# Kernel optimization log

Hardware: AMD Instinct MI355X
Metric: run time of the kernel (lower is better)

Reference implementation:

```python
import jax, jax.numpy as jnp
import numpy as np

MAX_ITERS = 20
TOL = 1e-6
STEP = 1.0
EPS = 1e-7
CLIP = 1e-7


def _normalize(x, axis=-1):
    n = jnp.linalg.norm(x, axis=axis, keepdims=True)
    return x / jnp.maximum(n, 1e-12)


def _safe_acos(x):
    return jnp.arccos(jnp.clip(x, -1.0 + CLIP, 1.0 - CLIP))


def setup_inputs() -> dict:
    key = jax.random.key(0)
    NC, K, N, D = 1000, 8, 32, 128
    X_groups = jax.random.normal(key, (NC, K, N, D), dtype=jnp.float32)
    return {"X_groups": X_groups}


def reference(X_groups):
    # X_groups: (NC, K, N, D)
    NC, K, N, D = X_groups.shape
    X = X_groups.reshape(NC * K, N, D)
    Xn = _normalize(X)                      # (G, N, D) unit vectors
    mu = _normalize(jnp.mean(Xn, axis=1))   # (G, D) init mean

    done = jnp.array(False)
    for _ in range(MAX_ITERS):
        dots = jnp.einsum('gd,gnd->gn', mu, Xn)             # (G, N)
        theta = _safe_acos(dots)
        sin_t = jnp.maximum(jnp.sin(theta), EPS)
        diff = Xn - dots[..., None] * mu[:, None, :]        # (G, N, D)
        log_vecs = (theta / sin_t)[..., None] * diff        # log map
        v = jnp.mean(log_vecs, axis=1)                      # (G, D)
        v_norm = jnp.maximum(jnp.linalg.norm(v, axis=-1, keepdims=True), EPS)
        done = done | (jnp.max(v_norm) < TOL)               # global convergence (as in torch .item() check)
        v_step = STEP * v
        vs_norm = jnp.maximum(jnp.linalg.norm(v_step, axis=-1, keepdims=True), EPS)
        mu_new = jnp.cos(vs_norm) * mu + jnp.sin(vs_norm) * (v_step / vs_norm)  # exp map
        mu_new = _normalize(mu_new)
        mu = jnp.where(done, mu, mu_new)

    # calc_cluster_distance: features (G, N, D) @ means (G, D)
    sims = jnp.einsum('gnd,gd->gn', Xn, mu)
    sims = jnp.clip(sims, -1 + CLIP, 1 - CLIP)
    loss = jnp.mean(jnp.sum(jnp.arccos(sims) ** 2, axis=-1))
    return loss
```

## Files before the change

kernel.cpp:

```cpp
#include <hip/hip_runtime.h>
#include <stdint.h>

#define MAX_ITERS 20
#define EPSV 1e-7f
#define CLIPV 1e-7f
#define PI_F 3.14159265358979f
#define PIO2_F 1.57079632679490f

typedef __attribute__((ext_vector_type(8))) short short8;
typedef __attribute__((ext_vector_type(4))) float f4;

__device__ __forceinline__ f4 mfma_bf16(short8 a, short8 b, f4 c) {
    return __builtin_amdgcn_mfma_f32_16x16x32_bf16(a, b, c, 0, 0, 0);
}

__device__ __forceinline__ float rl(float v, int l) {
    return __int_as_float(__builtin_amdgcn_readlane(__float_as_int(v), l));
}

template <int CTRL>
__device__ __forceinline__ float dpp_add(float v) {
    int p = __builtin_amdgcn_update_dpp(0, __float_as_int(v), CTRL, 0xF, 0xF, true);
    return v + __int_as_float(p);
}

__device__ __forceinline__ float rowsum32(float v) {
    v = dpp_add<0xB1>(v);
    v = dpp_add<0x4E>(v);
    v = dpp_add<0x141>(v);
    v = dpp_add<0x140>(v);
    return rl(v, 0) + rl(v, 16);
}

__device__ __forceinline__ float fast_acos(float x) {
    float a = fabsf(x);
    bool big = a > 0.5f;
    float z = big ? 0.5f * (1.0f - a) : x * x;
    float s = big ? sqrtf(z) : x;
    float p = fmaf(z, fmaf(z, fmaf(z, fmaf(z, 4.2163199048e-2f, 2.4181311049e-2f),
                                   4.5470025998e-2f), 7.4953002686e-2f),
                   1.6666752422e-1f);
    float r = fmaf(s * z, p, s);
    float big_val = (x < 0.0f) ? (PI_F - 2.0f * r) : (2.0f * r);
    return big ? big_val : (PIO2_F - r);
}

__device__ __forceinline__ void cvt_hilo(const float* v, short8& hi, short8& lo) {
#pragma unroll
    for (int i = 0; i < 8; ++i) {
        float x = v[i];
        uint32_t u = __float_as_uint(x);
        float hf = __uint_as_float(u & 0xFFFF0000u);
        float lf = x - hf;
        hi[i] = (short)(u >> 16);
        lo[i] = (short)(__float_as_uint(lf) >> 16);
    }
}

__global__ void __launch_bounds__(256) karcher(const float* __restrict__ X,
                                               float* __restrict__ ws,
                                               int n_groups) {
    __shared__ float sG[4][32 * 33];
    __shared__ float sInv[4][32];
    __shared__ float sPart[4];

    const int lane = threadIdx.x & 63;
    const int wid  = threadIdx.x >> 6;
    const int g    = blockIdx.x * 4 + wid;
    if (g >= n_groups) return;

    const float* Xg = X + (size_t)g * (32 * 128);
    const int col  = lane & 15;
    const int quad = lane >> 4;

    f4 acc00 = {0.f, 0.f, 0.f, 0.f};
    f4 acc01 = acc00, acc10 = acc00, acc11 = acc00;
#pragma unroll
    for (int kc = 0; kc < 4; ++kc) {
        const float* p0 = Xg + col * 128 + kc * 32 + quad * 8;
        const float* p1 = p0 + 16 * 128;
        float r0[8], r1[8];
        *(float4*)(r0)     = *(const float4*)(p0);
        *(float4*)(r0 + 4) = *(const float4*)(p0 + 4);
        *(float4*)(r1)     = *(const float4*)(p1);
        *(float4*)(r1 + 4) = *(const float4*)(p1 + 4);
        short8 H0, L0, H1, L1;
        cvt_hilo(r0, H0, L0);
        cvt_hilo(r1, H1, L1);
        acc00 = mfma_bf16(H0, H0, acc00);
        acc00 = mfma_bf16(H0, L0, acc00);
        acc00 = mfma_bf16(L0, H0, acc00);
        acc01 = mfma_bf16(H0, H1, acc01);
        acc01 = mfma_bf16(H0, L1, acc01);
        acc01 = mfma_bf16(L0, H1, acc01);
        acc10 = mfma_bf16(H1, H0, acc10);
        acc10 = mfma_bf16(H1, L0, acc10);
        acc10 = mfma_bf16(L1, H0, acc10);
        acc11 = mfma_bf16(H1, H1, acc11);
        acc11 = mfma_bf16(H1, L1, acc11);
        acc11 = mfma_bf16(L1, H1, acc11);
    }

    float* Gw = sG[wid];
#pragma unroll
    for (int i = 0; i < 4; ++i) {
        int rw = quad * 4 + i;
        Gw[rw * 33 + col]             = acc00[i];
        Gw[rw * 33 + col + 16]        = acc01[i];
        Gw[(rw + 16) * 33 + col]      = acc10[i];
        Gw[(rw + 16) * 33 + col + 16] = acc11[i];
    }
    __syncthreads();

    const int r = lane & 31;
    {
        float d = Gw[r * 33 + r];
        sInv[wid][r] = 1.0f / fmaxf(sqrtf(d), 1e-12f);
    }
    __syncthreads();

    float Grow[32];
    {
        float invr = sInv[wid][r];
#pragma unroll
        for (int j = 0; j < 32; ++j)
            Grow[j] = Gw[r * 33 + j] * (invr * sInv[wid][j]);
    }

    float a = 1.0f / 32.0f;
    float ga;
    {
        float s0 = 0, s1 = 0, s2 = 0, s3 = 0;
#pragma unroll
        for (int j = 0; j < 8; ++j) {
            s0 += Grow[j];
            s1 += Grow[j + 8];
            s2 += Grow[j + 16];
            s3 += Grow[j + 24];
        }
        ga = ((s0 + s1) + (s2 + s3)) * (1.0f / 32.0f);
        float n2   = rowsum32(a * ga);
        float inv0 = 1.0f / fmaxf(sqrtf(n2), 1e-12f);
        a  *= inv0;
        ga *= inv0;
    }

    for (int it = 0; it < MAX_ITERS; ++it) {
        float x  = fminf(fmaxf(ga, -1.0f + CLIPV), 1.0f - CLIPV);
        float th = fast_acos(x);
        float st = fmaxf(sqrtf(fmaxf(1.0f - x * x, 0.0f)), EPSV);
        float w  = __fdividef(th, st);
        float C  = rowsum32(w * ga);
        float beta = (w - C * a) * (1.0f / 32.0f);
        float gb0 = 0, gb1 = 0, gb2 = 0, gb3 = 0;
#pragma unroll
        for (int j = 0; j < 8; ++j) {
            gb0 = fmaf(Grow[j],      rl(beta, j),      gb0);
            gb1 = fmaf(Grow[j + 8],  rl(beta, j + 8),  gb1);
            gb2 = fmaf(Grow[j + 16], rl(beta, j + 16), gb2);
            gb3 = fmaf(Grow[j + 24], rl(beta, j + 24), gb3);
        }
        float gb = (gb0 + gb1) + (gb2 + gb3);
        float vv = rowsum32(beta * gb);
        float vs = fmaxf(sqrtf(fmaxf(vv, 0.0f)), EPSV);
        float cv = __cosf(vs);
        float sv = __fdividef(__sinf(vs), vs);
        a  = fmaf(sv, beta, cv * a);
        ga = fmaf(sv, gb, cv * ga);
        if (vs < 1e-6f) break;
    }

    float xf = fminf(fmaxf(ga, -1.0f + CLIPV), 1.0f - CLIPV);
    float t  = fast_acos(xf);
    float ls = rowsum32(t * t);
    if (lane == 0) sPart[wid] = ls;
    __syncthreads();
    if (threadIdx.x == 0)
        ws[blockIdx.x] = (sPart[0] + sPart[1]) + (sPart[2] + sPart[3]);
}

__global__ void __launch_bounds__(256) reduce_partials(const float* __restrict__ ws,
                                                       float* __restrict__ out,
                                                       int n, float scale) {
    __shared__ float sred[4];
    float s = 0.f;
    for (int i = threadIdx.x; i < n; i += 256) s += ws[i];
#pragma unroll
    for (int m = 32; m >= 1; m >>= 1) s += __shfl_xor(s, m, 64);
    const int lane = threadIdx.x & 63, wid = threadIdx.x >> 6;
    if (lane == 0) sred[wid] = s;
    __syncthreads();
    if (threadIdx.x == 0)
        out[0] = ((sred[0] + sred[1]) + (sred[2] + sred[3])) * scale;
}

extern "C" void kernel_launch(void* const* d_in, const int* in_sizes, int n_in,
                              void* d_out, int out_size, void* d_ws, size_t ws_size,
                              hipStream_t stream) {
    const float* X = (const float*)d_in[0];
    float* out = (float*)d_out;
    float* ws = (float*)d_ws;
    int n_groups = in_sizes[0] / (32 * 128);
    int blocks = (n_groups + 3) / 4;
    karcher<<<blocks, 256, 0, stream>>>(X, ws, n_groups);
    reduce_partials<<<1, 256, 0, stream>>>(ws, out, blocks, 1.0f / (float)n_groups);
}
```

Before: 211.0 us.

## Process two groups per wavefront using both 32-lane halves in the iteration

```diff
diff --git a/kernel.cpp b/kernel.cpp
--- a/kernel.cpp
+++ b/kernel.cpp
@@ -14,22 +14,23 @@
     return __builtin_amdgcn_mfma_f32_16x16x32_bf16(a, b, c, 0, 0, 0);
 }
 
-__device__ __forceinline__ float rl(float v, int l) {
-    return __int_as_float(__builtin_amdgcn_readlane(__float_as_int(v), l));
-}
-
 template <int CTRL>
 __device__ __forceinline__ float dpp_add(float v) {
     int p = __builtin_amdgcn_update_dpp(0, __float_as_int(v), CTRL, 0xF, 0xF, true);
     return v + __int_as_float(p);
 }
 
-__device__ __forceinline__ float rowsum32(float v) {
+__device__ __forceinline__ float halfsum32(float v) {
     v = dpp_add<0xB1>(v);
     v = dpp_add<0x4E>(v);
     v = dpp_add<0x141>(v);
     v = dpp_add<0x140>(v);
-    return rl(v, 0) + rl(v, 16);
+    int sw = __builtin_amdgcn_ds_swizzle(__float_as_int(v), 0x401F);
+    return v + __int_as_float(sw);
+}
+
+__device__ __forceinline__ float bperm(int addr, int src) {
+    return __int_as_float(__builtin_amdgcn_ds_bpermute(addr, src));
 }
 
 __device__ __forceinline__ float fast_acos(float x) {
@@ -57,74 +58,82 @@
     }
 }
 
-__global__ void __launch_bounds__(256) karcher(const float* __restrict__ X,
-                                               float* __restrict__ ws,
-                                               int n_groups) {
-    __shared__ float sG[4][32 * 33];
-    __shared__ float sInv[4][32];
-    __shared__ float sPart[4];
+__global__ void __launch_bounds__(256, 4) karcher(const float* __restrict__ X,
+                                                  float* __restrict__ ws,
+                                                  int n_groups) {
+    __shared__ float sG[8][32 * 33];
+    __shared__ float sPart[8];
 
     const int lane = threadIdx.x & 63;
     const int wid  = threadIdx.x >> 6;
-    const int g    = blockIdx.x * 4 + wid;
-    if (g >= n_groups) return;
-
-    const float* Xg = X + (size_t)g * (32 * 128);
+    const int g0   = blockIdx.x * 8 + wid * 2;
+    if (threadIdx.x < 8) sPart[threadIdx.x] = 0.f;
+    if (g0 >= n_groups) return;
+
     const int col  = lane & 15;
     const int quad = lane >> 4;
 
-    f4 acc00 = {0.f, 0.f, 0.f, 0.f};
-    f4 acc01 = acc00, acc10 = acc00, acc11 = acc00;
-#pragma unroll
-    for (int kc = 0; kc < 4; ++kc) {
-        const float* p0 = Xg + col * 128 + kc * 32 + quad * 8;
-        const float* p1 = p0 + 16 * 128;
-        float r0[8], r1[8];
-        *(float4*)(r0)     = *(const float4*)(p0);
-        *(float4*)(r0 + 4) = *(const float4*)(p0 + 4);
-        *(float4*)(r1)     = *(const float4*)(p1);
-        *(float4*)(r1 + 4) = *(const float4*)(p1 + 4);
-        short8 H0, L0, H1, L1;
-        cvt_hilo(r0, H0, L0);
-        cvt_hilo(r1, H1, L1);
-        acc00 = mfma_bf16(H0, H0, acc00);
-        acc00 = mfma_bf16(H0, L0, acc00);
-        acc00 = mfma_bf16(L0, H0, acc00);
-        acc01 = mfma_bf16(H0, H1, acc01);
-        acc01 = mfma_bf16(H0, L1, acc01);
-        acc01 = mfma_bf16(L0, H1, acc01);
-        acc10 = mfma_bf16(H1, H0, acc10);
-        acc10 = mfma_bf16(H1, L0, acc10);
-        acc10 = mfma_bf16(L1, H0, acc10);
-        acc11 = mfma_bf16(H1, H1, acc11);
-        acc11 = mfma_bf16(H1, L1, acc11);
-        acc11 = mfma_bf16(L1, H1, acc11);
-    }
-
-    float* Gw = sG[wid];
-#pragma unroll
-    for (int i = 0; i < 4; ++i) {
-        int rw = quad * 4 + i;
-        Gw[rw * 33 + col]             = acc00[i];
-        Gw[rw * 33 + col + 16]        = acc01[i];
-        Gw[(rw + 16) * 33 + col]      = acc10[i];
-        Gw[(rw + 16) * 33 + col + 16] = acc11[i];
+#pragma unroll
+    for (int gg = 0; gg < 2; ++gg) {
+        if (g0 + gg >= n_groups) break;
+        const float* Xg = X + (size_t)(g0 + gg) * (32 * 128);
+        f4 acc00 = {0.f, 0.f, 0.f, 0.f};
+        f4 acc01 = acc00, acc10 = acc00, acc11 = acc00;
+#pragma unroll
+        for (int kc = 0; kc < 4; ++kc) {
+            const float* p0 = Xg + col * 128 + kc * 32 + quad * 8;
+            const float* p1 = p0 + 16 * 128;
+            float r0[8], r1[8];
+            *(float4*)(r0)     = *(const float4*)(p0);
+            *(float4*)(r0 + 4) = *(const float4*)(p0 + 4);
+            *(float4*)(r1)     = *(const float4*)(p1);
+            *(float4*)(r1 + 4) = *(const float4*)(p1 + 4);
+            short8 H0, L0, H1, L1;
+            cvt_hilo(r0, H0, L0);
+            cvt_hilo(r1, H1, L1);
+            acc00 = mfma_bf16(H0, H0, acc00);
+            acc00 = mfma_bf16(H0, L0, acc00);
+            acc00 = mfma_bf16(L0, H0, acc00);
+            acc01 = mfma_bf16(H0, H1, acc01);
+            acc01 = mfma_bf16(H0, L1, acc01);
+            acc01 = mfma_bf16(L0, H1, acc01);
+            acc10 = mfma_bf16(H1, H0, acc10);
+            acc10 = mfma_bf16(H1, L0, acc10);
+            acc10 = mfma_bf16(L1, H0, acc10);
+            acc11 = mfma_bf16(H1, H1, acc11);
+            acc11 = mfma_bf16(H1, L1, acc11);
+            acc11 = mfma_bf16(L1, H1, acc11);
+        }
+        float* Gw = sG[wid * 2 + gg];
+#pragma unroll
+        for (int i = 0; i < 4; ++i) {
+            int rw = quad * 4 + i;
+            Gw[rw * 33 + col]             = acc00[i];
+            Gw[rw * 33 + col + 16]        = acc01[i];
+            Gw[(rw + 16) * 33 + col]      = acc10[i];
+            Gw[(rw + 16) * 33 + col + 16] = acc11[i];
+        }
     }
     __syncthreads();
 
-    const int r = lane & 31;
-    {
-        float d = Gw[r * 33 + r];
-        sInv[wid][r] = 1.0f / fmaxf(sqrtf(d), 1e-12f);
-    }
-    __syncthreads();
+    const int half = lane >> 5;
+    const int r    = lane & 31;
+    const float* Gh = sG[wid * 2 + half];
+
+    const int bbase = (lane & 32) << 2;
+    int badr[32];
+#pragma unroll
+    for (int j = 0; j < 32; ++j) badr[j] = bbase | (j << 2);
+
+    float d   = Gh[r * 34];
+    float inv = 1.0f / fmaxf(sqrtf(d), 1e-12f);
+    const int invb = __float_as_int(inv);
 
     float Grow[32];
-    {
-        float invr = sInv[wid][r];
-#pragma unroll
-        for (int j = 0; j < 32; ++j)
-            Grow[j] = Gw[r * 33 + j] * (invr * sInv[wid][j]);
+#pragma unroll
+    for (int j = 0; j < 32; ++j) {
+        float invj = bperm(badr[j], invb);
+        Grow[j] = Gh[r * 33 + j] * (inv * invj);
     }
 
     float a = 1.0f / 32.0f;
@@ -139,7 +148,7 @@
             s3 += Grow[j + 24];
         }
         ga = ((s0 + s1) + (s2 + s3)) * (1.0f / 32.0f);
-        float n2   = rowsum32(a * ga);
+        float n2   = halfsum32(a * ga);
         float inv0 = 1.0f / fmaxf(sqrtf(n2), 1e-12f);
         a  *= inv0;
         ga *= inv0;
@@ -150,33 +159,38 @@
         float th = fast_acos(x);
         float st = fmaxf(sqrtf(fmaxf(1.0f - x * x, 0.0f)), EPSV);
         float w  = __fdividef(th, st);
-        float C  = rowsum32(w * ga);
+        float C  = halfsum32(w * ga);
         float beta = (w - C * a) * (1.0f / 32.0f);
+        const int bi = __float_as_int(beta);
         float gb0 = 0, gb1 = 0, gb2 = 0, gb3 = 0;
 #pragma unroll
         for (int j = 0; j < 8; ++j) {
-            gb0 = fmaf(Grow[j],      rl(beta, j),      gb0);
-            gb1 = fmaf(Grow[j + 8],  rl(beta, j + 8),  gb1);
-            gb2 = fmaf(Grow[j + 16], rl(beta, j + 16), gb2);
-            gb3 = fmaf(Grow[j + 24], rl(beta, j + 24), gb3);
+            gb0 = fmaf(Grow[j],      bperm(badr[j],      bi), gb0);
+            gb1 = fmaf(Grow[j + 8],  bperm(badr[j + 8],  bi), gb1);
+            gb2 = fmaf(Grow[j + 16], bperm(badr[j + 16], bi), gb2);
+            gb3 = fmaf(Grow[j + 24], bperm(badr[j + 24], bi), gb3);
         }
         float gb = (gb0 + gb1) + (gb2 + gb3);
-        float vv = rowsum32(beta * gb);
+        float vv = halfsum32(beta * gb);
         float vs = fmaxf(sqrtf(fmaxf(vv, 0.0f)), EPSV);
         float cv = __cosf(vs);
         float sv = __fdividef(__sinf(vs), vs);
         a  = fmaf(sv, beta, cv * a);
         ga = fmaf(sv, gb, cv * ga);
-        if (vs < 1e-6f) break;
+        if (__all(vs < 1e-6f)) break;
     }
 
     float xf = fminf(fmaxf(ga, -1.0f + CLIPV), 1.0f - CLIPV);
     float t  = fast_acos(xf);
-    float ls = rowsum32(t * t);
-    if (lane == 0) sPart[wid] = ls;
+    float ls = halfsum32(t * t);
+    if (r == 0 && (g0 + half) < n_groups) sPart[wid * 2 + half] = ls;
     __syncthreads();
-    if (threadIdx.x == 0)
-        ws[blockIdx.x] = (sPart[0] + sPart[1]) + (sPart[2] + sPart[3]);
+    if (threadIdx.x == 0) {
+        float s = 0.f;
+#pragma unroll
+        for (int i = 0; i < 8; ++i) s += sPart[i];
+        ws[blockIdx.x] = s;
+    }
 }
 
 __global__ void __launch_bounds__(256) reduce_partials(const float* __restrict__ ws,
@@ -201,7 +215,7 @@
     float* out = (float*)d_out;
     float* ws = (float*)d_ws;
     int n_groups = in_sizes[0] / (32 * 128);
-    int blocks = (n_groups + 3) / 4;
+    int blocks = (n_groups + 7) / 8;
     karcher<<<blocks, 256, 0, stream>>>(X, ws, n_groups);
     reduce_partials<<<1, 256, 0, stream>>>(ws, out, blocks, 1.0f / (float)n_groups);
 }
```

New measurement: 217.9 us. +3.3%, slower.
